# Optimization experiments

Measured on AMD Instinct MI355X. Metric: run time of the kernel, lower is better.

Reference implementation:

```python
import jax, jax.numpy as jnp
import numpy as np

N_HEAD = 16
ROPE_BASE = 10000.0


def _rope(x, cos, sin):
    # x: [B,H,T,D]; cos/sin: [T,D/2] broadcast over B,H
    half = x.shape[-1] // 2
    x1, x2 = x[..., :half], x[..., half:]
    return jnp.concatenate([x1 * cos - x2 * sin, x1 * sin + x2 * cos], axis=-1)


def setup_inputs() -> dict:
    key = jax.random.key(0)
    k1, k2, k3 = jax.random.split(key, 3)
    C = 2048
    x = jax.random.normal(k1, (4, 2048, C), dtype=jnp.float32)
    w_qkv = jax.random.normal(k2, (C, 3 * C), dtype=jnp.float32) * 0.02
    w_proj = jax.random.normal(k3, (C, C), dtype=jnp.float32) * 0.02
    return {"x": x, "w_qkv": w_qkv, "w_proj": w_proj}


def reference(x, w_qkv, w_proj):
    B, T, C = x.shape
    H = N_HEAD
    D = C // H
    half = D // 2

    qkv = x @ w_qkv  # [B,T,3C]
    q, k, v = jnp.split(qkv, 3, axis=-1)
    # [B,T,C] -> [B,H,T,D]
    q = q.reshape(B, T, H, D).transpose(0, 2, 1, 3)
    k = k.reshape(B, T, H, D).transpose(0, 2, 1, 3)
    v = v.reshape(B, T, H, D).transpose(0, 2, 1, 3)

    # RoPE cache (start_pos = 0, no kv_cache / prefill path)
    inv_freq = 1.0 / (ROPE_BASE ** (jnp.arange(half, dtype=jnp.float32) / half))
    pos = jnp.arange(T, dtype=jnp.float32)
    freqs = pos[:, None] * inv_freq[None, :]  # [T, half]
    cos, sin = jnp.cos(freqs), jnp.sin(freqs)

    q = _rope(q, cos, sin)
    k = _rope(k, cos, sin)

    # scaled dot-product attention with explicit causal mask
    att = jnp.einsum("bhqd,bhkd->bhqk", q, k) / jnp.sqrt(jnp.asarray(D, x.dtype))
    causal = jnp.arange(T)[:, None] >= jnp.arange(T)[None, :]  # [T,T] bool
    att = jnp.where(causal, att, jnp.asarray(-jnp.inf, att.dtype))
    att = jax.nn.softmax(att, axis=-1)
    # dropout = identity (eval mode)
    out = jnp.einsum("bhqk,bhkd->bhqd", att, v)
    out = out.transpose(0, 2, 1, 3).reshape(B, T, C)
    out = out @ w_proj
    return out, k, v  # (output, new kv-cache)
```

## Files before the change

### kernel.cpp

```cpp
#include <hip/hip_runtime.h>
#include <math.h>

#define CDIM 2048
#define TDIM 2048
#define BDIM 4
#define HDIM 16
#define DDIM 128
#define M1   (BDIM * TDIM)
#define N1   (3 * CDIM)
#define KK   CDIM
#define NT   32

typedef unsigned short u16;
typedef __bf16 bf16x8 __attribute__((ext_vector_type(8)));
typedef float f32x4 __attribute__((ext_vector_type(4)));

__device__ __forceinline__ u16 f2b(float f) {
  union { float f; unsigned u; } x; x.f = f;
  unsigned r = x.u + 0x7fffu + ((x.u >> 16) & 1u);
  return (u16)(r >> 16);
}

__device__ __forceinline__ void gload_lds16(const void* g, void* l) {
  __builtin_amdgcn_global_load_lds(
      (__attribute__((address_space(1))) void*)g,
      (__attribute__((address_space(3))) void*)l, 16, 0, 0);
}

__global__ void convert_x(const float* __restrict__ x, u16* __restrict__ xb, int n4) {
  int i = blockIdx.x * blockDim.x + threadIdx.x;
  if (i < n4) {
    float4 v = ((const float4*)x)[i];
    unsigned long long o = (unsigned long long)f2b(v.x)
                         | ((unsigned long long)f2b(v.y) << 16)
                         | ((unsigned long long)f2b(v.z) << 32)
                         | ((unsigned long long)f2b(v.w) << 48);
    ((unsigned long long*)xb)[i] = o;
  }
}

__global__ void transpose_w(const float* __restrict__ w, u16* __restrict__ wt, int K, int N) {
  __shared__ float tile[32][33];
  const int n0 = blockIdx.x * 32, k0 = blockIdx.y * 32;
  const int tx = threadIdx.x & 31, ty = threadIdx.x >> 5;
  for (int r = ty; r < 32; r += 8)
    tile[r][tx] = w[(k0 + r) * N + n0 + tx];
  __syncthreads();
  for (int r = ty; r < 32; r += 8)
    wt[(n0 + r) * K + k0 + tx] = f2b(tile[tx][r]);
}

__global__ void rope_tab(float* __restrict__ cosT, float* __restrict__ sinT) {
  int i = blockIdx.x * blockDim.x + threadIdx.x;
  int t = i >> 6, d = i & 63;
  double inv = pow(10000.0, -(double)d / 64.0);
  double a = (double)t * inv;
  cosT[i] = (float)cos(a);
  sinT[i] = (float)sin(a);
}

__global__ void transpose_v(const float* __restrict__ v, u16* __restrict__ vt) {
  __shared__ float tile[32][33];
  const int bh = blockIdx.z;
  const int t0 = blockIdx.x * 32, d0 = blockIdx.y * 32;
  const int tx = threadIdx.x & 31, ty = threadIdx.x >> 5;
  const float* src = v + (bh * TDIM + t0) * DDIM + d0;
  for (int r = ty; r < 32; r += 8)
    tile[r][tx] = src[r * DDIM + tx];
  __syncthreads();
  u16* dst = vt + (bh * DDIM + d0) * TDIM + t0;
  for (int r = ty; r < 32; r += 8)
    dst[r * TDIM + tx] = f2b(tile[tx][r]);
}


#define VMW4 asm volatile("s_waitcnt vmcnt(4)" ::: "memory");
#define VMW2 asm volatile("s_waitcnt vmcnt(2)" ::: "memory");
#define VMW0 asm volatile("s_waitcnt vmcnt(0)" ::: "memory");
#define NOWAIT

#define GEMM256_ITER(bufA_, bufB_, nA_, nB_, kno_, STG, W0, W1, W3)            \
  {                                                                            \
    bf16x8 afr[4][2], bfr[2][2], bfr2[2][2];                                   \
      \
    _Pragma("unroll")                                                          \
    for (int i = 0; i < 4; ++i)                                                \
      _Pragma("unroll")                                                        \
      for (int kh = 0; kh < 2; ++kh)                                           \
        afr[i][kh] = *(const bf16x8*)&(bufA_)[aoff + i * 1024 +                \
                                              (((kh * 4 + quad) ^ rsw) * 8)];  \
    _Pragma("unroll")                                                          \
    for (int j = 0; j < 2; ++j)                                                \
      _Pragma("unroll")                                                        \
      for (int kh = 0; kh < 2; ++kh)                                           \
        bfr[j][kh] = *(const bf16x8*)&(bufB_)[boff + j * 1024 +                \
                                              (((kh * 4 + quad) ^ rsw) * 8)];  \
    if (STG) {                                                                 \
      _Pragma("unroll")                                                        \
      for (int q = 0; q < 2; ++q)                                              \
        gload_lds16(AgBase + (q * 128) * KK + (kno_),                          \
                    &(nA_)[q * 4096 + ldsw]);                                  \
    }                                                                          \
    __builtin_amdgcn_s_barrier();                                              \
    asm volatile("s_waitcnt lgkmcnt(0)" ::: "memory");                         \
    __builtin_amdgcn_s_setprio(1);                                             \
    _Pragma("unroll")                                                          \
    for (int i = 0; i < 4; ++i)                                                \
      _Pragma("unroll")                                                        \
      for (int j = 0; j < 2; ++j)                                              \
        _Pragma("unroll")                                                      \
        for (int kh = 0; kh < 2; ++kh)                                         \
          acc[i][j] = __builtin_amdgcn_mfma_f32_16x16x32_bf16(                 \
              afr[i][kh], bfr[j][kh], acc[i][j], 0, 0, 0);                     \
    __builtin_amdgcn_s_setprio(0);                                             \
    W0                                                                         \
    __builtin_amdgcn_s_barrier();                                              \
      \
    _Pragma("unroll")                                                          \
    for (int j = 0; j < 2; ++j)                                                \
      _Pragma("unroll")                                                        \
      for (int kh = 0; kh < 2; ++kh)                                           \
        bfr2[j][kh] = *(const bf16x8*)&(bufB_)[8192 + boff + j * 1024 +        \
                                               (((kh * 4 + quad) ^ rsw) * 8)]; \
    if (STG) {                                                                 \
      _Pragma("unroll")                                                        \
      for (int q = 0; q < 2; ++q)                                              \
        gload_lds16(BgBase + (q * 128) * KK + (kno_),                          \
                    &(nB_)[q * 4096 + ldsw]);                                  \
    }                                                                          \
    __builtin_amdgcn_s_barrier();                                              \
    asm volatile("s_waitcnt lgkmcnt(0)" ::: "memory");                         \
    __builtin_amdgcn_s_setprio(1);                                             \
    _Pragma("unroll")                                                          \
    for (int i = 0; i < 4; ++i)                                                \
      _Pragma("unroll")                                                        \
      for (int j = 0; j < 2; ++j)                                              \
        _Pragma("unroll")                                                      \
        for (int kh = 0; kh < 2; ++kh)                                         \
          acc[i][2 + j] = __builtin_amdgcn_mfma_f32_16x16x32_bf16(             \
              afr[i][kh], bfr2[j][kh], acc[i][2 + j], 0, 0, 0);                \
    __builtin_amdgcn_s_setprio(0);                                             \
    W1                                                                         \
    __builtin_amdgcn_s_barrier();                                              \
      \
    _Pragma("unroll")                                                          \
    for (int i = 0; i < 4; ++i)                                                \
      _Pragma("unroll")                                                        \
      for (int kh = 0; kh < 2; ++kh)                                           \
        afr[i][kh] = *(const bf16x8*)&(bufA_)[8192 + aoff + i * 1024 +         \
                                              (((kh * 4 + quad) ^ rsw) * 8)];  \
    if (STG) {                                                                 \
      _Pragma("unroll")                                                        \
      for (int q = 0; q < 2; ++q)                                              \
        gload_lds16(BgBase + (q * 128 + 32) * KK + (kno_),                     \
                    &(nB_)[8192 + q * 4096 + ldsw]);                           \
    }                                                                          \
    __builtin_amdgcn_s_barrier();                                              \
    asm volatile("s_waitcnt lgkmcnt(0)" ::: "memory");                         \
    __builtin_amdgcn_s_setprio(1);                                             \
    _Pragma("unroll")                                                          \
    for (int i = 0; i < 4; ++i)                                                \
      _Pragma("unroll")                                                        \
      for (int j = 0; j < 2; ++j)                                              \
        _Pragma("unroll")                                                      \
        for (int kh = 0; kh < 2; ++kh)                                         \
          acc[4 + i][2 + j] = __builtin_amdgcn_mfma_f32_16x16x32_bf16(         \
              afr[i][kh], bfr2[j][kh], acc[4 + i][2 + j], 0, 0, 0);            \
    __builtin_amdgcn_s_setprio(0);                                             \
    __builtin_amdgcn_s_barrier();                                              \
      \
    _Pragma("unroll")                                                          \
    for (int j = 0; j < 2; ++j)                                                \
      _Pragma("unroll")                                                        \
      for (int kh = 0; kh < 2; ++kh)                                           \
        bfr[j][kh] = *(const bf16x8*)&(bufB_)[boff + j * 1024 +                \
                                              (((kh * 4 + quad) ^ rsw) * 8)];  \
    if (STG) {                                                                 \
      _Pragma("unroll")                                                        \
      for (int q = 0; q < 2; ++q)                                              \
        gload_lds16(AgBase + (q * 128 + 64) * KK + (kno_),                     \
                    &(nA_)[8192 + q * 4096 + ldsw]);                           \
    }                                                                          \
    __builtin_amdgcn_s_barrier();                                              \
    asm volatile("s_waitcnt lgkmcnt(0)" ::: "memory");                         \
    __builtin_amdgcn_s_setprio(1);                                             \
    _Pragma("unroll")                                                          \
    for (int i = 0; i < 4; ++i)                                                \
      _Pragma("unroll")                                                        \
      for (int j = 0; j < 2; ++j)                                              \
        _Pragma("unroll")                                                      \
        for (int kh = 0; kh < 2; ++kh)                                         \
          acc[4 + i][j] = __builtin_amdgcn_mfma_f32_16x16x32_bf16(             \
              afr[i][kh], bfr[j][kh], acc[4 + i][j], 0, 0, 0);                 \
    __builtin_amdgcn_s_setprio(0);                                             \
    W3                                                                         \
    __builtin_amdgcn_s_barrier();                                              \
  }

#define GEMM256_MAINLOOP(APTR, BPTR)                                           \
  const int rA = lane >> 3, cA = lane & 7;                                     \
  const int w8r = wave * 8 + rA;                                               \
  const int swz8 = (cA ^ rA) * 8;                                              \
  const u16* AgBase = (APTR) + (m0 + w8r) * KK + swz8;                         \
  const int nb = ((w8r >> 5) * 64) + (w8r & 31);                               \
  const u16* BgBase = (BPTR) + (n0 + nb) * KK + swz8;                          \
  const int ldsw = wave * 512;                                                 \
  const int rsw = c16 & 7;                                                     \
  const int aoff = (((wave >> 2) * 64) + c16) * 64;                            \
  const int boff = (((wave & 3) * 32) + c16) * 64;                             \
  f32x4 acc[8][4];                                                             \
  {                                                                            \
    f32x4 z = {0.f, 0.f, 0.f, 0.f};                                            \
    _Pragma("unroll")                                                          \
    for (int i = 0; i < 8; ++i)                                                \
      _Pragma("unroll")                                                        \
      for (int j = 0; j < 4; ++j) acc[i][j] = z;                               \
  }                                                                            \
                  \
  _Pragma("unroll")                                                            \
  for (int q = 0; q < 2; ++q)                                                  \
    gload_lds16(AgBase + (q * 128) * KK, &lds[q * 4096 + ldsw]);               \
  _Pragma("unroll")                                                            \
  for (int q = 0; q < 2; ++q)                                                  \
    gload_lds16(BgBase + (q * 128) * KK, &lds[32768 + q * 4096 + ldsw]);       \
  _Pragma("unroll")                                                            \
  for (int q = 0; q < 2; ++q)                                                  \
    gload_lds16(BgBase + (q * 128 + 32) * KK,                                  \
                &lds[32768 + 8192 + q * 4096 + ldsw]);                         \
  _Pragma("unroll")                                                            \
  for (int q = 0; q < 2; ++q)                                                  \
    gload_lds16(AgBase + (q * 128 + 64) * KK, &lds[8192 + q * 4096 + ldsw]);   \
  VMW4                                                                         \
  __builtin_amdgcn_s_barrier();                                                \
  for (int kt = 0; kt < NT - 1; ++kt) {                                        \
    const int cur = kt & 1;                                                    \
    const u16* bA = &lds[cur * 16384];                                         \
    const u16* bB = &lds[32768 + cur * 16384];                                 \
    u16* nA = &lds[(cur ^ 1) * 16384];                                         \
    u16* nB = &lds[32768 + (cur ^ 1) * 16384];                                 \
    const int kno = (kt + 1) * 64;                                             \
    GEMM256_ITER(bA, bB, nA, nB, kno, 1, VMW4, VMW4, VMW4)                     \
  }                                                                            \
                    \
  GEMM256_ITER((&lds[16384]), (&lds[32768 + 16384]), (&lds[0]),                \
               (&lds[32768]), 0, 0, VMW2, VMW0, NOWAIT)

__global__ __launch_bounds__(512, 2) void gemm_qkv(
    const u16* __restrict__ A,
    const u16* __restrict__ Bt,
    const float* __restrict__ cosT, const float* __restrict__ sinT,
    u16* __restrict__ qb, u16* __restrict__ kb,
    float* __restrict__ kout, float* __restrict__ vout)
{
  extern __shared__ __align__(16) u16 lds[];
  const int tid = threadIdx.x, wave = tid >> 6, lane = tid & 63;
  const int quad = lane >> 4, c16 = lane & 15;
  const int bid = blockIdx.y * 24 + blockIdx.x;
  const int swz = (bid & 7) * 96 + (bid >> 3);
  const int m0 = (swz / 24) * 256, n0 = (swz % 24) * 256;
  const int wm = (wave >> 2) * 128, wn = (wave & 3) * 64;
  (void)wm; (void)wn;

  GEMM256_MAINLOOP(A, Bt)

  float* cbuf = (float*)lds;
  const int mat = n0 >> 11;
  const int hbase = (n0 & 2047) >> 7;
  const float qscale = 0.088388347648318447f;
#pragma unroll
  for (int pass = 0; pass < 4; ++pass) {
    __syncthreads();
    if ((wave >> 2) == (pass >> 1)) {
#pragma unroll
      for (int i = 0; i < 4; ++i) {
        const int mf = (pass & 1) * 4 + i;
#pragma unroll
        for (int j = 0; j < 4; ++j)
#pragma unroll
          for (int r = 0; r < 4; ++r)
            cbuf[(i * 16 + quad * 4 + r) * 260 + (wave & 3) * 64 + j * 16 + c16] = acc[mf][j][r];
      }
    }
    __syncthreads();
#pragma unroll
    for (int it = 0; it < 16; ++it) {
      int p = it * 512 + tid;
      int lr = p >> 7;
      int hc = (p >> 6) & 1;
      int d = p & 63;
      float x1 = cbuf[lr * 260 + hc * 128 + d];
      float x2 = cbuf[lr * 260 + hc * 128 + 64 + d];
      int mg = m0 + pass * 64 + lr;
      int b = mg >> 11, t = mg & 2047;
      int h = hbase + hc;
      int idx = ((b * HDIM + h) * TDIM + t) * DDIM + d;
      if (mat == 2) {
        vout[idx] = x1; vout[idx + 64] = x2;
      } else {
        float cs = cosT[t * 64 + d], sn = sinT[t * 64 + d];
        float o1 = x1 * cs - x2 * sn;
        float o2 = x1 * sn + x2 * cs;
        if (mat == 0) {
          qb[idx] = f2b(o1 * qscale); qb[idx + 64] = f2b(o2 * qscale);
        } else {
          kout[idx] = o1; kout[idx + 64] = o2;
          kb[idx] = f2b(o1); kb[idx + 64] = f2b(o2);
        }
      }
    }
  }
}

__global__ __launch_bounds__(512, 2) void gemm_proj(
    const u16* __restrict__ A,
    const u16* __restrict__ Bt,
    float* __restrict__ out)
{
  extern __shared__ __align__(16) u16 lds[];
  const int tid = threadIdx.x, wave = tid >> 6, lane = tid & 63;
  const int quad = lane >> 4, c16 = lane & 15;
  const int bid = blockIdx.y * 8 + blockIdx.x;
  const int swz = (bid & 7) * 32 + (bid >> 3);
  const int m0 = (swz >> 3) * 256, n0 = (swz & 7) * 256;
  const int wm = (wave >> 2) * 128, wn = (wave & 3) * 64;

  GEMM256_MAINLOOP(A, Bt)

#pragma unroll
  for (int mf = 0; mf < 8; ++mf)
#pragma unroll
    for (int nf = 0; nf < 4; ++nf)
#pragma unroll
      for (int r = 0; r < 4; ++r)
        out[(m0 + wm + mf * 16 + quad * 4 + r) * CDIM + n0 + wn + nf * 16 + c16] =
            acc[mf][nf][r];
}

__global__ __launch_bounds__(256, 2) void attn(
    const u16* __restrict__ qb, const u16* __restrict__ kb,
    const u16* __restrict__ vt, u16* __restrict__ att)
{
  __shared__ __attribute__((aligned(16))) u16 sh[24576];
  u16* const ksm = sh;
  u16* const vsm = sh + 8192;
  u16* const psm = sh + 16384;

  const int tid = threadIdx.x, wave = tid >> 6, lane = tid & 63;
  const int quad = lane >> 4, c16 = lane & 15;
  const int bx = blockIdx.x;
  const int bh = blockIdx.y;

  for (int hv = 0; hv < 2; ++hv) {
    const int qt = hv ? (7 - bx) : (bx + 8);
    const int q0 = qt * 128;

    {
      const u16* qg = qb + (bh * TDIM + q0) * DDIM;
      const int rowl = wave * 4 + (lane >> 4);
      const int ch = lane & 15;
#pragma unroll
      for (int r = 0; r < 8; ++r) {
        int row = r * 16 + rowl;
        gload_lds16(qg + row * DDIM + (ch ^ (row & 15)) * 8,
                    &sh[(r * 16 + wave * 4) * 128]);
      }
    }
    __syncthreads();
    bf16x8 qf[2][4];
#pragma unroll
    for (int g = 0; g < 2; ++g)
#pragma unroll
      for (int kp = 0; kp < 4; ++kp)
        qf[g][kp] = *(const bf16x8*)&sh[(g * 64 + wave * 16 + c16) * 128 +
                                        (((kp * 4 + quad) ^ c16) * 8)];
    __syncthreads();

    f32x4 o[2][8];
    f32x4 zero = {0.f, 0.f, 0.f, 0.f};
#pragma unroll
    for (int g = 0; g < 2; ++g)
#pragma unroll
      for (int jd = 0; jd < 8; ++jd) o[g][jd] = zero;
    float mrow[2][4], lrow[2][4];
#pragma unroll
    for (int g = 0; g < 2; ++g)
#pragma unroll
      for (int r = 0; r < 4; ++r) { mrow[g][r] = -INFINITY; lrow[g][r] = 0.f; }

    const int nchunk = 2 * qt + 2;
    for (int kc = 0; kc < nchunk; ++kc) {
      const int kc0 = kc * 64;
      {
        const u16* kg = kb + (bh * TDIM + kc0) * DDIM;
        const int rowl = wave * 4 + (lane >> 4);
        const int ch = lane & 15;
#pragma unroll
        for (int r = 0; r < 4; ++r) {
          int row = r * 16 + rowl;
          gload_lds16(kg + row * DDIM + (ch ^ (row & 15)) * 8,
                      &ksm[(r * 16 + wave * 4) * 128]);
        }
        const u16* vg = vt + bh * (DDIM * TDIM) + kc0;
        const int rowv = wave * 8 + (lane >> 3);
        const int chv = lane & 7;
#pragma unroll
        for (int r = 0; r < 4; ++r) {
          int row = r * 32 + rowv;
          gload_lds16(vg + row * TDIM + (chv ^ (row & 7)) * 8,
                      &vsm[(r * 32 + wave * 8) * 64]);
        }
      }
      __syncthreads();

      f32x4 st[2][4];
#pragma unroll
      for (int g = 0; g < 2; ++g)
#pragma unroll
        for (int j = 0; j < 4; ++j) st[g][j] = zero;
#pragma unroll
      for (int kp = 0; kp < 4; ++kp) {
#pragma unroll
        for (int j = 0; j < 4; ++j) {
          bf16x8 bk = *(const bf16x8*)&ksm[(j * 16 + c16) * 128 +
                                           (((kp * 4 + quad) ^ c16) * 8)];
          st[0][j] = __builtin_amdgcn_mfma_f32_16x16x32_bf16(qf[0][kp], bk, st[0][j], 0, 0, 0);
          st[1][j] = __builtin_amdgcn_mfma_f32_16x16x32_bf16(qf[1][kp], bk, st[1][j], 0, 0, 0);
        }
      }

      u16* const pw = psm + wave * 2048;
      float al2[2][4];
#pragma unroll
      for (int g = 0; g < 2; ++g) {
        const bool dg = (kc >= 2 * qt + g);
        const int qrow_base = q0 + g * 64 + wave * 16 + quad * 4;
#pragma unroll
        for (int r = 0; r < 4; ++r) {
          float mx = -INFINITY;
#pragma unroll
          for (int j = 0; j < 4; ++j) {
            float sv = st[g][j][r];
            if (dg && (kc0 + j * 16 + c16 > qrow_base + r)) sv = -INFINITY;
            st[g][j][r] = sv;
            mx = fmaxf(mx, sv);
          }
          mx = fmaxf(mx, __shfl_xor(mx, 1, 64));
          mx = fmaxf(mx, __shfl_xor(mx, 2, 64));
          mx = fmaxf(mx, __shfl_xor(mx, 4, 64));
          mx = fmaxf(mx, __shfl_xor(mx, 8, 64));
          float mnew = fmaxf(mrow[g][r], mx);
          float al = __expf(mrow[g][r] - mnew);
          mrow[g][r] = mnew;
          al2[g][r] = al;
          float sum = 0.f;
          const int row16 = quad * 4 + r;
#pragma unroll
          for (int j = 0; j < 4; ++j) {
            float p = __expf(st[g][j][r] - mnew);
            sum += p;
            int chunk = (j * 2 + (c16 >> 3)) ^ (row16 & 7);
            pw[g * 1024 + row16 * 64 + chunk * 8 + (c16 & 7)] = f2b(p);
          }
          sum += __shfl_xor(sum, 1, 64);
          sum += __shfl_xor(sum, 2, 64);
          sum += __shfl_xor(sum, 4, 64);
          sum += __shfl_xor(sum, 8, 64);
          lrow[g][r] = lrow[g][r] * al + sum;
        }
#pragma unroll
        for (int jd = 0; jd < 8; ++jd)
#pragma unroll
          for (int r = 0; r < 4; ++r)
            o[g][jd][r] *= al2[g][r];
      }

      asm volatile("s_waitcnt lgkmcnt(0)" ::: "memory");

#pragma unroll
      for (int s = 0; s < 2; ++s) {
        const int chp = ((s * 4 + quad) ^ (c16 & 7)) * 8;
        bf16x8 ap0 = *(const bf16x8*)&pw[c16 * 64 + chp];
        bf16x8 ap1 = *(const bf16x8*)&pw[1024 + c16 * 64 + chp];
#pragma unroll
        for (int jd = 0; jd < 8; ++jd) {
          bf16x8 bv = *(const bf16x8*)&vsm[(jd * 16 + c16) * 64 + chp];
          o[0][jd] = __builtin_amdgcn_mfma_f32_16x16x32_bf16(ap0, bv, o[0][jd], 0, 0, 0);
          o[1][jd] = __builtin_amdgcn_mfma_f32_16x16x32_bf16(ap1, bv, o[1][jd], 0, 0, 0);
        }
      }
      __syncthreads();
    }

    const int b = bh >> 4, h = bh & 15;
#pragma unroll
    for (int g = 0; g < 2; ++g) {
      float ri[4];
#pragma unroll
      for (int r = 0; r < 4; ++r) ri[r] = 1.f / lrow[g][r];
#pragma unroll
      for (int jd = 0; jd < 8; ++jd)
#pragma unroll
        for (int r = 0; r < 4; ++r) {
          int t = q0 + g * 64 + wave * 16 + quad * 4 + r;
          att[(b * TDIM + t) * CDIM + h * DDIM + jd * 16 + c16] = f2b(o[g][jd][r] * ri[r]);
        }
    }
  }
}

extern "C" void kernel_launch(void* const* d_in, const int* in_sizes, int n_in,
                              void* d_out, int out_size, void* d_ws, size_t ws_size,
                              hipStream_t stream) {
  (void)in_sizes; (void)n_in; (void)out_size; (void)ws_size;
  const float* x      = (const float*)d_in[0];
  const float* w_qkv  = (const float*)d_in[1];
  const float* w_proj = (const float*)d_in[2];
  float* out  = (float*)d_out;
  float* kout = out + 16777216;
  float* vout = out + 2 * 16777216;

  char* ws = (char*)d_ws;
  u16*   xb     = (u16*)(ws);
  u16*   wqkvT  = (u16*)(ws + 33554432);
  u16*   wprojT = (u16*)(ws + 58720256);
  float* cosT   = (float*)(ws + 67108864);
  float* sinT   = (float*)(ws + 67633152);
  u16*   qb     = (u16*)(ws + 68157440);
  u16*   kb     = (u16*)(ws + 101711872);
  u16*   vt     = (u16*)(ws + 135266304);
  u16*   att    = xb;

  static int attr_set = 0;
  if (!attr_set) {
    hipFuncSetAttribute((const void*)gemm_qkv,
                        hipFuncAttributeMaxDynamicSharedMemorySize, 131072);
    hipFuncSetAttribute((const void*)gemm_proj,
                        hipFuncAttributeMaxDynamicSharedMemorySize, 131072);
    attr_set = 1;
  }

  convert_x<<<16384, 256, 0, stream>>>(x, xb, 4194304);
  transpose_w<<<dim3(192, 64), 256, 0, stream>>>(w_qkv, wqkvT, KK, N1);
  transpose_w<<<dim3(64, 64), 256, 0, stream>>>(w_proj, wprojT, KK, CDIM);
  rope_tab<<<512, 256, 0, stream>>>(cosT, sinT);
  gemm_qkv<<<dim3(24, 32), 512, 131072, stream>>>(xb, wqkvT, cosT, sinT, qb, kb, kout, vout);
  transpose_v<<<dim3(64, 4, 64), 256, 0, stream>>>(vout, vt);
  attn<<<dim3(8, 64), 256, 0, stream>>>(qb, kb, vt, att);
  gemm_proj<<<dim3(8, 32), 512, 131072, stream>>>(att, wprojT, out);
}
```

Before: 767.2 us.

## Restructure GEMM k-step to double-buffer fragment registers and cut barriers

Rewrites the 256x256 GEMM inner step so A and B fragments for the second half live in separate registers (aX/aY, bX/bY). Each LDS read can then be issued before the previous MFMA block finishes, and most per-quarter barriers and lgkmcnt waits are dropped. Global-to-LDS prefetches are moved after the MFMA blocks and the vmcnt waits are retuned. Launch bounds drop to one block per CU to make room for the extra registers, which lowers occupancy. Removing barriers also risks LDS read/write hazards between waves.

```diff
diff --git a/kernel.cpp b/kernel.cpp
--- a/kernel.cpp
+++ b/kernel.cpp
@@ -79,30 +79,24 @@
 #define VMW0 asm volatile("s_waitcnt vmcnt(0)" ::: "memory");
 #define NOWAIT
 
-#define GEMM256_ITER(bufA_, bufB_, nA_, nB_, kno_, STG, W0, W1, W3)            \
+#define GEMM256_TILE(bufA_, bufB_, nA_, nB_, kno_, STG, W2, WEND)              \
   {                                                                            \
-    bf16x8 afr[4][2], bfr[2][2], bfr2[2][2];                                   \
-      \
+    __builtin_amdgcn_s_barrier();        \
+    bf16x8 aX[4][2], aY[4][2], bX[2][2], bY[2][2];                             \
+                                  \
     _Pragma("unroll")                                                          \
     for (int i = 0; i < 4; ++i)                                                \
       _Pragma("unroll")                                                        \
       for (int kh = 0; kh < 2; ++kh)                                           \
-        afr[i][kh] = *(const bf16x8*)&(bufA_)[aoff + i * 1024 +                \
-                                              (((kh * 4 + quad) ^ rsw) * 8)];  \
+        aX[i][kh] = *(const bf16x8*)&(bufA_)[aoff + i * 1024 +                 \
+                                             (((kh * 4 + quad) ^ rsw) * 8)];   \
     _Pragma("unroll")                                                          \
     for (int j = 0; j < 2; ++j)                                                \
       _Pragma("unroll")                                                        \
       for (int kh = 0; kh < 2; ++kh)                                           \
-        bfr[j][kh] = *(const bf16x8*)&(bufB_)[boff + j * 1024 +                \
-                                              (((kh * 4 + quad) ^ rsw) * 8)];  \
-    if (STG) {                                                                 \
-      _Pragma("unroll")                                                        \
-      for (int q = 0; q < 2; ++q)                                              \
-        gload_lds16(AgBase + (q * 128) * KK + (kno_),                          \
-                    &(nA_)[q * 4096 + ldsw]);                                  \
-    }                                                                          \
-    __builtin_amdgcn_s_barrier();                                              \
-    asm volatile("s_waitcnt lgkmcnt(0)" ::: "memory");                         \
+        bX[j][kh] = *(const bf16x8*)&(bufB_)[boff + j * 1024 +                 \
+                                             (((kh * 4 + quad) ^ rsw) * 8)];   \
+                                                         \
     __builtin_amdgcn_s_setprio(1);                                             \
     _Pragma("unroll")                                                          \
     for (int i = 0; i < 4; ++i)                                                \
@@ -111,25 +105,26 @@
         _Pragma("unroll")                                                      \
         for (int kh = 0; kh < 2; ++kh)                                         \
           acc[i][j] = __builtin_amdgcn_mfma_f32_16x16x32_bf16(                 \
-              afr[i][kh], bfr[j][kh], acc[i][j], 0, 0, 0);                     \
+              aX[i][kh], bX[j][kh], acc[i][j], 0, 0, 0);                       \
     __builtin_amdgcn_s_setprio(0);                                             \
-    W0                                                                         \
-    __builtin_amdgcn_s_barrier();                                              \
-      \
-    _Pragma("unroll")                                                          \
-    for (int j = 0; j < 2; ++j)                                                \
-      _Pragma("unroll")                                                        \
-      for (int kh = 0; kh < 2; ++kh)                                           \
-        bfr2[j][kh] = *(const bf16x8*)&(bufB_)[8192 + boff + j * 1024 +        \
-                                               (((kh * 4 + quad) ^ rsw) * 8)]; \
     if (STG) {                                                                 \
+      _Pragma("unroll")                                                        \
+      for (int q = 0; q < 2; ++q)                                              \
+        gload_lds16(AgBase + (q * 128) * KK + (kno_), &(nA_)[q * 4096 + ldsw]);\
       _Pragma("unroll")                                                        \
       for (int q = 0; q < 2; ++q)                                              \
         gload_lds16(BgBase + (q * 128) * KK + (kno_),                          \
                     &(nB_)[q * 4096 + ldsw]);                                  \
     }                                                                          \
-    __builtin_amdgcn_s_barrier();                                              \
-    asm volatile("s_waitcnt lgkmcnt(0)" ::: "memory");                         \
+    _Pragma("unroll")                                                          \
+    for (int j = 0; j < 2; ++j)                                                \
+      _Pragma("unroll")                                                        \
+      for (int kh = 0; kh < 2; ++kh)                                           \
+        bY[j][kh] = *(const bf16x8*)&(bufB_)[8192 + boff + j * 1024 +          \
+                                             (((kh * 4 + quad) ^ rsw) * 8)];   \
+    W2                                                                         \
+    __builtin_amdgcn_s_barrier();                       \
+                                                         \
     __builtin_amdgcn_s_setprio(1);                                             \
     _Pragma("unroll")                                                          \
     for (int i = 0; i < 4; ++i)                                                \
@@ -138,25 +133,21 @@
         _Pragma("unroll")                                                      \
         for (int kh = 0; kh < 2; ++kh)                                         \
           acc[i][2 + j] = __builtin_amdgcn_mfma_f32_16x16x32_bf16(             \
-              afr[i][kh], bfr2[j][kh], acc[i][2 + j], 0, 0, 0);                \
+              aX[i][kh], bY[j][kh], acc[i][2 + j], 0, 0, 0);                   \
     __builtin_amdgcn_s_setprio(0);                                             \
-    W1                                                                         \
-    __builtin_amdgcn_s_barrier();                                              \
-      \
-    _Pragma("unroll")                                                          \
-    for (int i = 0; i < 4; ++i)                                                \
-      _Pragma("unroll")                                                        \
-      for (int kh = 0; kh < 2; ++kh)                                           \
-        afr[i][kh] = *(const bf16x8*)&(bufA_)[8192 + aoff + i * 1024 +         \
-                                              (((kh * 4 + quad) ^ rsw) * 8)];  \
     if (STG) {                                                                 \
       _Pragma("unroll")                                                        \
       for (int q = 0; q < 2; ++q)                                              \
         gload_lds16(BgBase + (q * 128 + 32) * KK + (kno_),                     \
                     &(nB_)[8192 + q * 4096 + ldsw]);                           \
     }                                                                          \
-    __builtin_amdgcn_s_barrier();                                              \
-    asm volatile("s_waitcnt lgkmcnt(0)" ::: "memory");                         \
+    _Pragma("unroll")                                                          \
+    for (int i = 0; i < 4; ++i)                                                \
+      _Pragma("unroll")                                                        \
+      for (int kh = 0; kh < 2; ++kh)                                           \
+        aY[i][kh] = *(const bf16x8*)&(bufA_)[8192 + aoff + i * 1024 +          \
+                                             (((kh * 4 + quad) ^ rsw) * 8)];   \
+                                                         \
     __builtin_amdgcn_s_setprio(1);                                             \
     _Pragma("unroll")                                                          \
     for (int i = 0; i < 4; ++i)                                                \
@@ -165,24 +156,21 @@
         _Pragma("unroll")                                                      \
         for (int kh = 0; kh < 2; ++kh)                                         \
           acc[4 + i][2 + j] = __builtin_amdgcn_mfma_f32_16x16x32_bf16(         \
-              afr[i][kh], bfr2[j][kh], acc[4 + i][2 + j], 0, 0, 0);            \
+              aY[i][kh], bY[j][kh], acc[4 + i][2 + j], 0, 0, 0);               \
     __builtin_amdgcn_s_setprio(0);                                             \
-    __builtin_amdgcn_s_barrier();                                              \
-      \
-    _Pragma("unroll")                                                          \
-    for (int j = 0; j < 2; ++j)                                                \
-      _Pragma("unroll")                                                        \
-      for (int kh = 0; kh < 2; ++kh)                                           \
-        bfr[j][kh] = *(const bf16x8*)&(bufB_)[boff + j * 1024 +                \
-                                              (((kh * 4 + quad) ^ rsw) * 8)];  \
     if (STG) {                                                                 \
       _Pragma("unroll")                                                        \
       for (int q = 0; q < 2; ++q)                                              \
         gload_lds16(AgBase + (q * 128 + 64) * KK + (kno_),                     \
                     &(nA_)[8192 + q * 4096 + ldsw]);                           \
     }                                                                          \
-    __builtin_amdgcn_s_barrier();                                              \
-    asm volatile("s_waitcnt lgkmcnt(0)" ::: "memory");                         \
+    _Pragma("unroll")                                                          \
+    for (int j = 0; j < 2; ++j)                                                \
+      _Pragma("unroll")                                                        \
+      for (int kh = 0; kh < 2; ++kh)                                           \
+        bX[j][kh] = *(const bf16x8*)&(bufB_)[boff + j * 1024 +                 \
+                                             (((kh * 4 + quad) ^ rsw) * 8)];   \
+                                                         \
     __builtin_amdgcn_s_setprio(1);                                             \
     _Pragma("unroll")                                                          \
     for (int i = 0; i < 4; ++i)                                                \
@@ -191,10 +179,9 @@
         _Pragma("unroll")                                                      \
         for (int kh = 0; kh < 2; ++kh)                                         \
           acc[4 + i][j] = __builtin_amdgcn_mfma_f32_16x16x32_bf16(             \
-              afr[i][kh], bfr[j][kh], acc[4 + i][j], 0, 0, 0);                 \
+              aY[i][kh], bX[j][kh], acc[4 + i][j], 0, 0, 0);                   \
     __builtin_amdgcn_s_setprio(0);                                             \
-    W3                                                                         \
-    __builtin_amdgcn_s_barrier();                                              \
+    WEND                                                                       \
   }
 
 #define GEMM256_MAINLOOP(APTR, BPTR)                                           \
@@ -216,7 +203,7 @@
       _Pragma("unroll")                                                        \
       for (int j = 0; j < 4; ++j) acc[i][j] = z;                               \
   }                                                                            \
-                  \
+     \
   _Pragma("unroll")                                                            \
   for (int q = 0; q < 2; ++q)                                                  \
     gload_lds16(AgBase + (q * 128) * KK, &lds[q * 4096 + ldsw]);               \
@@ -230,8 +217,7 @@
   _Pragma("unroll")                                                            \
   for (int q = 0; q < 2; ++q)                                                  \
     gload_lds16(AgBase + (q * 128 + 64) * KK, &lds[8192 + q * 4096 + ldsw]);   \
-  VMW4                                                                         \
-  __builtin_amdgcn_s_barrier();                                                \
+  VMW2                                                                         \
   for (int kt = 0; kt < NT - 1; ++kt) {                                        \
     const int cur = kt & 1;                                                    \
     const u16* bA = &lds[cur * 16384];                                         \
@@ -239,13 +225,13 @@
     u16* nA = &lds[(cur ^ 1) * 16384];                                         \
     u16* nB = &lds[32768 + (cur ^ 1) * 16384];                                 \
     const int kno = (kt + 1) * 64;                                             \
-    GEMM256_ITER(bA, bB, nA, nB, kno, 1, VMW4, VMW4, VMW4)                     \
+    GEMM256_TILE(bA, bB, nA, nB, kno, 1, VMW4, VMW2)                           \
   }                                                                            \
-                    \
-  GEMM256_ITER((&lds[16384]), (&lds[32768 + 16384]), (&lds[0]),                \
-               (&lds[32768]), 0, 0, VMW2, VMW0, NOWAIT)
-
-__global__ __launch_bounds__(512, 2) void gemm_qkv(
+                 \
+  GEMM256_TILE((&lds[16384]), (&lds[32768 + 16384]), (&lds[0]),                \
+               (&lds[32768]), 0, 0, VMW0, NOWAIT)
+
+__global__ __launch_bounds__(512, 1) void gemm_qkv(
     const u16* __restrict__ A,
     const u16* __restrict__ Bt,
     const float* __restrict__ cosT, const float* __restrict__ sinT,
@@ -258,8 +244,6 @@
   const int bid = blockIdx.y * 24 + blockIdx.x;
   const int swz = (bid & 7) * 96 + (bid >> 3);
   const int m0 = (swz / 24) * 256, n0 = (swz % 24) * 256;
-  const int wm = (wave >> 2) * 128, wn = (wave & 3) * 64;
-  (void)wm; (void)wn;
 
   GEMM256_MAINLOOP(A, Bt)
 
@@ -311,7 +295,7 @@
   }
 }
 
-__global__ __launch_bounds__(512, 2) void gemm_proj(
+__global__ __launch_bounds__(512, 1) void gemm_proj(
     const u16* __restrict__ A,
     const u16* __restrict__ Bt,
     float* __restrict__ out)
@@ -322,10 +306,10 @@
   const int bid = blockIdx.y * 8 + blockIdx.x;
   const int swz = (bid & 7) * 32 + (bid >> 3);
   const int m0 = (swz >> 3) * 256, n0 = (swz & 7) * 256;
+
+  GEMM256_MAINLOOP(A, Bt)
+
   const int wm = (wave >> 2) * 128, wn = (wave & 3) * 64;
-
-  GEMM256_MAINLOOP(A, Bt)
-
 #pragma unroll
   for (int mf = 0; mf < 8; ++mf)
 #pragma unroll
```

Result: no change. 772.8 us (+0.7%).
